# Kernel tuning notes

Measured on AMD Instinct MI355X. Metric: run time of the kernel, lower is better.

The kernel has to match this reference:

```python
import jax, jax.numpy as jnp
import numpy as np

N, C, T, V = 128, 256, 48, 25
CR = C // 16
SEG = 3
BN_EPS = 1e-5


def setup_inputs() -> dict:
    key = jax.random.key(0)
    ks = jax.random.split(key, 8)
    s = lambda k, shape: jax.random.normal(k, shape, dtype=jnp.float32) * 0.05
    return {
        "x": jax.random.normal(ks[0], (N, C, T, V), dtype=jnp.float32),
        "w_sq": s(ks[1], (CR, C)),   # me_squeeze 1x1 conv weight [out,in]
        "b_sq": s(ks[2], (CR,)),
        "gamma": jnp.ones((CR,), jnp.float32),   # BN weight
        "beta": jnp.zeros((CR,), jnp.float32),   # BN bias
        "rmean": jnp.zeros((CR,), jnp.float32),  # BN running mean
        "rvar": jnp.ones((CR,), jnp.float32),    # BN running var
        "w_c1": s(ks[3], (CR, CR)),  # me_conv1 1x1 conv weight
        "b_c1": s(ks[4], (CR,)),
        "w_ex": s(ks[5], (C, CR)),   # me_expand 1x1 conv weight
        "b_ex": s(ks[6], (C,)),
    }


def reference(x, w_sq, b_sq, gamma, beta, rmean, rvar, w_c1, b_c1, w_ex, b_ex):
    n, c, t, v = x.shape
    nb = (n * t) // SEG
    cr = w_sq.shape[0]
    # 1x1 squeeze conv + BatchNorm (eval mode, running stats) -> [n, cr, t, v]
    y = jnp.einsum('nctv,rc->nrtv', x, w_sq) + b_sq[None, :, None, None]
    scale = gamma / jnp.sqrt(rvar + BN_EPS)
    y = y * scale[None, :, None, None] + (beta - rmean * scale)[None, :, None, None]
    # 1x1 conv on squeezed features (shifted branch)
    y1 = jnp.einsum('nrtv,sr->nstv', y, w_c1) + b_c1[None, :, None, None]
    # regroup consecutive frames into segments of SEG along time: (n*t) -> (nb, SEG)
    yseg = y.transpose(0, 2, 1, 3).reshape(nb, SEG, cr, v)
    y1seg = y1.transpose(0, 2, 1, 3).reshape(nb, SEG, cr, v)
    # temporal difference: conv(frame k+1) - frame k, zero-pad last frame of each segment
    diff = y1seg[:, 1:] - yseg[:, :SEG - 1]                    # [nb, SEG-1, cr, v]
    diff = jnp.pad(diff, ((0, 0), (0, 1), (0, 0), (0, 0)))     # [nb, SEG, cr, v]
    x_me = diff.reshape(n, t, cr, v).transpose(0, 2, 1, 3)     # [n, cr, t, v]
    # adaptive avg pool over joints (v -> 1), expand conv, sigmoid gate
    m = jnp.mean(x_me, axis=-1, keepdims=True)                 # [n, cr, t, 1]
    gate = jax.nn.sigmoid(jnp.einsum('nrtu,cr->nctu', m, w_ex) + b_ex[None, :, None, None])
    return x * gate
```

## Files before the change

### kernel.cpp

```cpp
#include <hip/hip_runtime.h>

#define N_  128
#define C_  256
#define T_  48
#define V_  25

__device__ __forceinline__ float b2f(unsigned short u) {
    union { float f; unsigned i; } c; c.i = ((unsigned)u) << 16; return c.f;
}
__device__ __forceinline__ unsigned short f2b(float f) {
    union { float f; unsigned i; } c; c.f = f;
    unsigned r = c.i + 0x7fffu + ((c.i >> 16) & 1u);
    return (unsigned short)(r >> 16);
}

__global__ __launch_bounds__(256, 3) void k_fused5(
    const float* __restrict__ x,
    const float* __restrict__ wsq, const float* __restrict__ bsq,
    const float* __restrict__ gamma, const float* __restrict__ beta,
    const float* __restrict__ rmean, const float* __restrict__ rvar,
    const float* __restrict__ wc1, const float* __restrict__ bc1,
    const float* __restrict__ wex, const float* __restrict__ bex,
    float* __restrict__ out)
{
    __shared__ unsigned short xs[256 * 78];
    __shared__ float xb[256 * 3];
    __shared__ float ybn[48];
    __shared__ float y1[48];
    __shared__ float mv[48];
    __shared__ float gs[256 * 3];

    const int tid = threadIdx.x;
    const unsigned bid = blockIdx.x;
    const unsigned o   = (bid & 7u) * 256u + (bid >> 3);
    const unsigned n   = o >> 4;
    const unsigned seg = o & 15u;

    const size_t nbase = (size_t)n * 307200u;
    const int a = (int)((seg * 75u) & 3u);
    const int h = (4 - a) & 3;
    const float* rowx = x   + nbase + seg * 75u;
    float*       rowo = out + nbase + seg * 75u;

    #pragma unroll
    for (int it = 0; it < 18; ++it) {
        int j = it * 256 + tid;
        int c = j / 18, k = j - c * 18;
        const float4 v = *(const float4*)(rowx + (unsigned)(c * 1200 + h + k * 4));
        unsigned p0 = (unsigned)f2b(v.x) | ((unsigned)f2b(v.y) << 16);
        unsigned p1 = (unsigned)f2b(v.z) | ((unsigned)f2b(v.w) << 16);
        unsigned s  = (unsigned)(c * 78 + k * 4);
        *(unsigned*)&xs[s]     = p0;
        *(unsigned*)&xs[s + 2] = p1;
    }
    {
        int j = tid;
        #pragma unroll
        for (int it = 0; it < 3; ++it, j += 256) {
            int c = j / 3, e = j - c * 3;
            int m = (e < h) ? e : e + 72;
            xs[c * 78 + 72 + e] = f2b(rowx[(unsigned)(c * 1200 + m)]);
        }
    }
    float wexr[16];
    #pragma unroll
    for (int r = 0; r < 16; ++r) wexr[r] = wex[tid * 16 + r];
    const float bexr = bex[tid];
    __syncthreads();

    {
        const int c = tid;
        float st[3] = {0.f, 0.f, 0.f};
        #pragma unroll
        for (int t = 0; t < 3; ++t) {
            #pragma unroll
            for (int v = 0; v < 25; ++v) {
                int m = t * 25 + v;
                int s = (m >= h && m < h + 72) ? (m - h) : ((m < h) ? 72 + m : m);
                st[t] += b2f(xs[c * 78 + s]);
            }
        }
        xb[c * 3 + 0] = st[0] * 0.04f;
        xb[c * 3 + 1] = st[1] * 0.04f;
        xb[c * 3 + 2] = st[2] * 0.04f;
    }
    __syncthreads();

    if (tid < 48) {
        const int tt = tid >> 4, r = tid & 15;
        float acc = 0.f;
        for (int c = 0; c < 256; ++c) acc += xb[c * 3 + tt] * wsq[r * 256 + c];
        float sc = gamma[r] * rsqrtf(rvar[r] + 1e-5f);
        ybn[tt * 16 + r] = (acc + bsq[r]) * sc + (beta[r] - rmean[r] * sc);
    }
    __syncthreads();
    if (tid < 48) {
        const int tt = tid >> 4, s = tid & 15;
        float acc = bc1[s];
        #pragma unroll
        for (int r = 0; r < 16; ++r) acc += ybn[tt * 16 + r] * wc1[s * 16 + r];
        y1[tt * 16 + s] = acc;
    }
    __syncthreads();
    if (tid < 48) {
        const int tt = tid >> 4, r = tid & 15;
        mv[tid] = (tt < 2) ? (y1[(tt + 1) * 16 + r] - ybn[tt * 16 + r]) : 0.f;
    }
    __syncthreads();
    {
        #pragma unroll
        for (int t = 0; t < 3; ++t) {
            float acc = bexr;
            #pragma unroll
            for (int r = 0; r < 16; ++r) acc += mv[t * 16 + r] * wexr[r];
            gs[tid * 3 + t] = 1.f / (1.f + expf(-acc));
        }
    }
    __syncthreads();

    #pragma unroll
    for (int it = 0; it < 18; ++it) {
        int j = it * 256 + tid;
        int c = j / 18, k = j - c * 18;
        unsigned s = (unsigned)(c * 78 + k * 4);
        unsigned q0 = *(const unsigned*)&xs[s];
        unsigned q1 = *(const unsigned*)&xs[s + 2];
        int m0  = h + k * 4;
        int t0  = (m0 * 41) >> 10;
        int rem = m0 - t0 * 25;
        float g0 = gs[c * 3 + t0];
        float g3 = gs[c * 3 + (((m0 + 3) * 41) >> 10)];
        float4 ov;
        ov.x = b2f((unsigned short)(q0 & 0xffffu)) * g0;
        ov.y = b2f((unsigned short)(q0 >> 16)) * ((rem + 1 < 25) ? g0 : g3);
        ov.z = b2f((unsigned short)(q1 & 0xffffu)) * ((rem + 2 < 25) ? g0 : g3);
        ov.w = b2f((unsigned short)(q1 >> 16)) * ((rem + 3 < 25) ? g0 : g3);
        *(float4*)(rowo + (unsigned)(c * 1200 + h + k * 4)) = ov;
    }
    {
        int j = tid;
        #pragma unroll
        for (int it = 0; it < 3; ++it, j += 256) {
            int c = j / 3, e = j - c * 3;
            int m = (e < h) ? e : e + 72;
            int t = (m * 41) >> 10;
            rowo[(unsigned)(c * 1200 + m)] = b2f(xs[c * 78 + 72 + e]) * gs[c * 3 + t];
        }
    }
}

extern "C" void kernel_launch(void* const* d_in, const int* in_sizes, int n_in,
                              void* d_out, int out_size, void* d_ws, size_t ws_size,
                              hipStream_t stream) {
    const float* x     = (const float*)d_in[0];
    const float* wsq   = (const float*)d_in[1];
    const float* bsq   = (const float*)d_in[2];
    const float* gamma = (const float*)d_in[3];
    const float* beta  = (const float*)d_in[4];
    const float* rmean = (const float*)d_in[5];
    const float* rvar  = (const float*)d_in[6];
    const float* wc1   = (const float*)d_in[7];
    const float* bc1   = (const float*)d_in[8];
    const float* wex   = (const float*)d_in[9];
    const float* bex   = (const float*)d_in[10];

    k_fused5<<<2048, 256, 0, stream>>>(x, wsq, bsq, gamma, beta,
                                       rmean, rvar, wc1, bc1, wex, bex,
                                       (float*)d_out);
}
```

Before: 89.26 us.

## Process four segments per block with register-prefetched next-segment loads

Each block now handles four consecutive time segments instead of one. It prefetches the next segment's x into registers while it computes the gate and writes the current segment. The squeeze weights and BN constants are staged in LDS once per block, and the squeeze reduction is split across 384 threads instead of 48. This trades fewer, longer-lived blocks and higher register and LDS pressure for overlap of global loads with the gate math and stores.

```diff
diff --git a/kernel.cpp b/kernel.cpp
--- a/kernel.cpp
+++ b/kernel.cpp
@@ -5,16 +5,37 @@
 #define T_  48
 #define V_  25
 
+typedef unsigned int u32;
+
 __device__ __forceinline__ float b2f(unsigned short u) {
-    union { float f; unsigned i; } c; c.i = ((unsigned)u) << 16; return c.f;
+    union { float f; u32 i; } c; c.i = ((u32)u) << 16; return c.f;
 }
 __device__ __forceinline__ unsigned short f2b(float f) {
-    union { float f; unsigned i; } c; c.f = f;
-    unsigned r = c.i + 0x7fffu + ((c.i >> 16) & 1u);
+    union { float f; u32 i; } c; c.f = f;
+    u32 r = c.i + 0x7fffu + ((c.i >> 16) & 1u);
     return (unsigned short)(r >> 16);
 }
 
-__global__ __launch_bounds__(256, 3) void k_fused5(
+template<int H>
+__device__ __forceinline__ void addSlot(float& s0, float& s1, float& s2, int s, float v) {
+    const int m = (s < 72) ? (s + H) : ((s - 72 < H) ? (s - 72) : s);
+    if (m < 25) s0 += v; else if (m < 50) s1 += v; else s2 += v;
+}
+
+template<int H>
+__device__ __forceinline__ void rowMeans(const unsigned short* row, float* xo) {
+    float s0 = 0.f, s1 = 0.f, s2 = 0.f;
+    #pragma unroll
+    for (int q = 0; q < 37; ++q) {
+        u32 u = *(const u32*)(row + 2 * q);
+        addSlot<H>(s0, s1, s2, 2 * q,     b2f((unsigned short)(u & 0xffffu)));
+        addSlot<H>(s0, s1, s2, 2 * q + 1, b2f((unsigned short)(u >> 16)));
+    }
+    addSlot<H>(s0, s1, s2, 74, b2f(row[74]));
+    xo[0] = s0 * 0.04f; xo[1] = s1 * 0.04f; xo[2] = s2 * 0.04f;
+}
+
+__global__ __launch_bounds__(256, 4) void k_pipe(
     const float* __restrict__ x,
     const float* __restrict__ wsq, const float* __restrict__ bsq,
     const float* __restrict__ gamma, const float* __restrict__ beta,
@@ -24,128 +45,172 @@
     float* __restrict__ out)
 {
     __shared__ unsigned short xs[256 * 78];
-    __shared__ float xb[256 * 3];
-    __shared__ float ybn[48];
-    __shared__ float y1[48];
-    __shared__ float mv[48];
-    __shared__ float gs[256 * 3];
+    __shared__ float wsqL[256 * 17];
+    __shared__ float wc1L[256];
+    __shared__ float xb[768];
+    __shared__ float gs[768];
+    __shared__ float ybn[48], y1[48], mv[48];
+    __shared__ float scL[16], shL[16], bc1L[16];
 
     const int tid = threadIdx.x;
     const unsigned bid = blockIdx.x;
-    const unsigned o   = (bid & 7u) * 256u + (bid >> 3);
-    const unsigned n   = o >> 4;
-    const unsigned seg = o & 15u;
-
-    const size_t nbase = (size_t)n * 307200u;
-    const int a = (int)((seg * 75u) & 3u);
-    const int h = (4 - a) & 3;
-    const float* rowx = x   + nbase + seg * 75u;
-    float*       rowo = out + nbase + seg * 75u;
-
-    #pragma unroll
-    for (int it = 0; it < 18; ++it) {
-        int j = it * 256 + tid;
-        int c = j / 18, k = j - c * 18;
-        const float4 v = *(const float4*)(rowx + (unsigned)(c * 1200 + h + k * 4));
-        unsigned p0 = (unsigned)f2b(v.x) | ((unsigned)f2b(v.y) << 16);
-        unsigned p1 = (unsigned)f2b(v.z) | ((unsigned)f2b(v.w) << 16);
-        unsigned s  = (unsigned)(c * 78 + k * 4);
-        *(unsigned*)&xs[s]     = p0;
-        *(unsigned*)&xs[s + 2] = p1;
-    }
-    {
-        int j = tid;
-        #pragma unroll
-        for (int it = 0; it < 3; ++it, j += 256) {
-            int c = j / 3, e = j - c * 3;
+    const unsigned o   = (bid & 7u) * 64u + (bid >> 3);
+    const unsigned n   = o >> 2;
+    const unsigned sq  = o & 3u;
+    const int seg0     = (int)(sq * 4);
+
+    const float* xn = x   + (size_t)n * 307200u;
+    float*       on = out + (size_t)n * 307200u;
+
+    float4 v[18]; float ev[3];
+
+    auto issueLoads = [&](int seg, int h) {
+        const float* rowx = xn + seg * 75;
+        #pragma unroll
+        for (int it = 0; it < 18; ++it) {
+            int j = it * 256 + tid, c = j / 18, k = j - c * 18;
+            v[it] = *(const float4*)(rowx + c * 1200 + h + k * 4);
+        }
+        #pragma unroll
+        for (int it = 0; it < 3; ++it) {
+            int j = it * 256 + tid, c = j / 3, e = j - c * 3;
             int m = (e < h) ? e : e + 72;
-            xs[c * 78 + 72 + e] = f2b(rowx[(unsigned)(c * 1200 + m)]);
-        }
-    }
-    float wexr[16];
-    #pragma unroll
-    for (int r = 0; r < 16; ++r) wexr[r] = wex[tid * 16 + r];
-    const float bexr = bex[tid];
-    __syncthreads();
-
-    {
-        const int c = tid;
-        float st[3] = {0.f, 0.f, 0.f};
-        #pragma unroll
-        for (int t = 0; t < 3; ++t) {
+            ev[it] = rowx[c * 1200 + m];
+        }
+    };
+    auto convertStore = [&]() {
+        #pragma unroll
+        for (int it = 0; it < 18; ++it) {
+            int j = it * 256 + tid, c = j / 18, k = j - c * 18;
+            u32 p0 = (u32)f2b(v[it].x) | ((u32)f2b(v[it].y) << 16);
+            u32 p1 = (u32)f2b(v[it].z) | ((u32)f2b(v[it].w) << 16);
+            u32 s  = (u32)(c * 78 + k * 4);
+            *(u32*)&xs[s]     = p0;
+            *(u32*)&xs[s + 2] = p1;
+        }
+        #pragma unroll
+        for (int it = 0; it < 3; ++it) {
+            int j = it * 256 + tid, c = j / 3, e = j - c * 3;
+            xs[c * 78 + 72 + e] = f2b(ev[it]);
+        }
+    };
+    auto gateMath = [&]() {
+        float* part = gs;
+        #pragma unroll
+        for (int pp = 0; pp < 2; ++pp) {
+            int p = pp * 256 + tid;
+            if (p < 384) {
+                int h8 = p / 48, q = p - h8 * 48, tt = q >> 4, r = q & 15;
+                float acc = 0.f;
+                #pragma unroll
+                for (int i = 0; i < 32; ++i)
+                    acc += xb[(h8 * 32 + i) * 3 + tt] * wsqL[(h8 * 32 + i) * 17 + r];
+                part[p] = acc;
+            }
+        }
+        __syncthreads();
+        if (tid < 48) {
+            int tt = tid >> 4, r = tid & 15;
+            float acc = 0.f;
             #pragma unroll
-            for (int v = 0; v < 25; ++v) {
-                int m = t * 25 + v;
-                int s = (m >= h && m < h + 72) ? (m - h) : ((m < h) ? 72 + m : m);
-                st[t] += b2f(xs[c * 78 + s]);
+            for (int h8 = 0; h8 < 8; ++h8) acc += part[h8 * 48 + tt * 16 + r];
+            ybn[tt * 16 + r] = acc * scL[r] + shL[r];
+        }
+        __syncthreads();
+        if (tid < 48) {
+            int tt = tid >> 4, s = tid & 15;
+            float acc = bc1L[s];
+            #pragma unroll
+            for (int r = 0; r < 16; ++r) acc += ybn[tt * 16 + r] * wc1L[s * 16 + r];
+            y1[tt * 16 + s] = acc;
+        }
+        __syncthreads();
+        if (tid < 48) {
+            int tt = tid >> 4, r = tid & 15;
+            mv[tid] = (tt < 2) ? (y1[(tt + 1) * 16 + r] - ybn[tt * 16 + r]) : 0.f;
+        }
+        __syncthreads();
+        {
+            float a0 = bex[tid], a1 = a0, a2 = a0;
+            #pragma unroll
+            for (int r = 0; r < 16; ++r) {
+                float wr = wex[tid * 16 + r];
+                a0 += mv[r]      * wr;
+                a1 += mv[16 + r] * wr;
+                a2 += mv[32 + r] * wr;
             }
-        }
-        xb[c * 3 + 0] = st[0] * 0.04f;
-        xb[c * 3 + 1] = st[1] * 0.04f;
-        xb[c * 3 + 2] = st[2] * 0.04f;
-    }
-    __syncthreads();
-
-    if (tid < 48) {
-        const int tt = tid >> 4, r = tid & 15;
-        float acc = 0.f;
-        for (int c = 0; c < 256; ++c) acc += xb[c * 3 + tt] * wsq[r * 256 + c];
-        float sc = gamma[r] * rsqrtf(rvar[r] + 1e-5f);
-        ybn[tt * 16 + r] = (acc + bsq[r]) * sc + (beta[r] - rmean[r] * sc);
-    }
-    __syncthreads();
-    if (tid < 48) {
-        const int tt = tid >> 4, s = tid & 15;
-        float acc = bc1[s];
-        #pragma unroll
-        for (int r = 0; r < 16; ++r) acc += ybn[tt * 16 + r] * wc1[s * 16 + r];
-        y1[tt * 16 + s] = acc;
-    }
-    __syncthreads();
-    if (tid < 48) {
-        const int tt = tid >> 4, r = tid & 15;
-        mv[tid] = (tt < 2) ? (y1[(tt + 1) * 16 + r] - ybn[tt * 16 + r]) : 0.f;
-    }
-    __syncthreads();
-    {
-        #pragma unroll
-        for (int t = 0; t < 3; ++t) {
-            float acc = bexr;
-            #pragma unroll
-            for (int r = 0; r < 16; ++r) acc += mv[t * 16 + r] * wexr[r];
-            gs[tid * 3 + t] = 1.f / (1.f + expf(-acc));
-        }
-    }
-    __syncthreads();
-
-    #pragma unroll
-    for (int it = 0; it < 18; ++it) {
-        int j = it * 256 + tid;
-        int c = j / 18, k = j - c * 18;
-        unsigned s = (unsigned)(c * 78 + k * 4);
-        unsigned q0 = *(const unsigned*)&xs[s];
-        unsigned q1 = *(const unsigned*)&xs[s + 2];
-        int m0  = h + k * 4;
-        int t0  = (m0 * 41) >> 10;
-        int rem = m0 - t0 * 25;
-        float g0 = gs[c * 3 + t0];
-        float g3 = gs[c * 3 + (((m0 + 3) * 41) >> 10)];
-        float4 ov;
-        ov.x = b2f((unsigned short)(q0 & 0xffffu)) * g0;
-        ov.y = b2f((unsigned short)(q0 >> 16)) * ((rem + 1 < 25) ? g0 : g3);
-        ov.z = b2f((unsigned short)(q1 & 0xffffu)) * ((rem + 2 < 25) ? g0 : g3);
-        ov.w = b2f((unsigned short)(q1 >> 16)) * ((rem + 3 < 25) ? g0 : g3);
-        *(float4*)(rowo + (unsigned)(c * 1200 + h + k * 4)) = ov;
-    }
-    {
-        int j = tid;
-        #pragma unroll
-        for (int it = 0; it < 3; ++it, j += 256) {
-            int c = j / 3, e = j - c * 3;
+            gs[tid * 3 + 0] = 1.f / (1.f + expf(-a0));
+            gs[tid * 3 + 1] = 1.f / (1.f + expf(-a1));
+            gs[tid * 3 + 2] = 1.f / (1.f + expf(-a2));
+        }
+        __syncthreads();
+    };
+    auto applyStore = [&](int seg, int h) {
+        float* rowo = on + seg * 75;
+        #pragma unroll
+        for (int it = 0; it < 18; ++it) {
+            int j = it * 256 + tid, c = j / 18, k = j - c * 18;
+            u32 s  = (u32)(c * 78 + k * 4);
+            u32 q0 = *(const u32*)&xs[s];
+            u32 q1 = *(const u32*)&xs[s + 2];
+            int m0 = h + k * 4;
+            int t0 = (m0 * 41) >> 10;
+            int rem = m0 - t0 * 25;
+            float g0 = gs[c * 3 + t0];
+            float g3 = gs[c * 3 + (((m0 + 3) * 41) >> 10)];
+            float4 ov;
+            ov.x = b2f((unsigned short)(q0 & 0xffffu)) * g0;
+            ov.y = b2f((unsigned short)(q0 >> 16))     * ((rem + 1 < 25) ? g0 : g3);
+            ov.z = b2f((unsigned short)(q1 & 0xffffu)) * ((rem + 2 < 25) ? g0 : g3);
+            ov.w = b2f((unsigned short)(q1 >> 16))     * ((rem + 3 < 25) ? g0 : g3);
+            *(float4*)(rowo + c * 1200 + h + k * 4) = ov;
+        }
+        #pragma unroll
+        for (int it = 0; it < 3; ++it) {
+            int j = it * 256 + tid, c = j / 3, e = j - c * 3;
             int m = (e < h) ? e : e + 72;
             int t = (m * 41) >> 10;
-            rowo[(unsigned)(c * 1200 + m)] = b2f(xs[c * 78 + 72 + e]) * gs[c * 3 + t];
-        }
+            rowo[c * 1200 + m] = b2f(xs[c * 78 + 72 + e]) * gs[c * 3 + t];
+        }
+    };
+
+    issueLoads(seg0, 0);
+    {
+        #pragma unroll
+        for (int it = 0; it < 16; ++it) {
+            int j = it * 256 + tid;
+            int r = j >> 8, c = j & 255;
+            wsqL[c * 17 + r] = wsq[j];
+        }
+        wc1L[tid] = wc1[tid];
+        if (tid < 16) {
+            float sc = gamma[tid] * rsqrtf(rvar[tid] + 1e-5f);
+            scL[tid] = sc;
+            shL[tid] = (beta[tid] - rmean[tid] * sc) + bsq[tid] * sc;
+            bc1L[tid] = bc1[tid];
+        }
+    }
+    convertStore();
+    __syncthreads();
+
+    #pragma unroll
+    for (int j = 0; j < 4; ++j) {
+        const int seg = seg0 + j;
+        if (j < 3) issueLoads(seg + 1, j + 1);
+        __builtin_amdgcn_sched_barrier(0);
+        {
+            const unsigned short* row = xs + tid * 78;
+            float* xo = xb + tid * 3;
+            if      (j == 0) rowMeans<0>(row, xo);
+            else if (j == 1) rowMeans<1>(row, xo);
+            else if (j == 2) rowMeans<2>(row, xo);
+            else             rowMeans<3>(row, xo);
+        }
+        __syncthreads();
+        gateMath();
+        applyStore(seg, j);
+        __syncthreads();
+        if (j < 3) { convertStore(); __syncthreads(); }
     }
 }
 
@@ -164,7 +229,7 @@
     const float* wex   = (const float*)d_in[9];
     const float* bex   = (const float*)d_in[10];
 
-    k_fused5<<<2048, 256, 0, stream>>>(x, wsq, bsq, gamma, beta,
-                                       rmean, rvar, wc1, bc1, wex, bex,
-                                       (float*)d_out);
-}
+    k_pipe<<<512, 256, 0, stream>>>(x, wsq, bsq, gamma, beta,
+                                    rmean, rvar, wc1, bc1, wex, bex,
+                                    (float*)d_out);
+}
```

Result: slower. 97.75 us (+9.5%).
